# Kernel tuning notes

Measured on AMD Instinct MI355X. Metric: run time of the kernel, lower is better.

Reference implementation:

```python
import jax, jax.numpy as jnp
import numpy as np

H = 16        # num_attention_heads
E = 1024      # hidden_size
D = E // H    # attention_head_size = 64
M = 1024      # max_position_embeddings
EPS = 1e-12


def setup_inputs() -> dict:
    key = jax.random.key(0)
    ks = jax.random.split(key, 12)
    s = 0.02
    B, S = 8, 1024
    return {
        "hidden_states": jax.random.normal(ks[0], (B, S, E), jnp.float32),
        "Wq": jax.random.normal(ks[1], (E, E), jnp.float32) * s,
        "bq": jnp.zeros((E,), jnp.float32),
        "Wk": jax.random.normal(ks[2], (E, E), jnp.float32) * s,
        "bk": jnp.zeros((E,), jnp.float32),
        "Wv": jax.random.normal(ks[3], (E, E), jnp.float32) * s,
        "bv": jnp.zeros((E,), jnp.float32),
        "dist_emb": jax.random.normal(ks[4], (2 * M - 1, D), jnp.float32) * s,
        "Wo": jax.random.normal(ks[5], (E, E), jnp.float32) * s,
        "bo": jnp.zeros((E,), jnp.float32),
        "ln_gamma": jnp.ones((E,), jnp.float32),
        "ln_beta": jnp.zeros((E,), jnp.float32),
    }


def reference(hidden_states, Wq, bq, Wk, bk, Wv, bv, dist_emb, Wo, bo, ln_gamma, ln_beta):
    B, S, _ = hidden_states.shape

    def heads(x):  # [B,S,E] -> [B,H,S,D]
        return x.reshape(B, S, H, D).transpose(0, 2, 1, 3)

    q = heads(hidden_states @ Wq + bq)
    k = heads(hidden_states @ Wk + bk)
    v = heads(hidden_states @ Wv + bv)

    scores = jnp.einsum("bhqd,bhkd->bhqk", q, k)

    # relative_key_query positional bias
    pos_l = jnp.arange(S)[:, None]
    pos_r = jnp.arange(S)[None, :]
    dist_idx = pos_l - pos_r + M - 1            # [S,S] in [0, 2M-2]
    pos_emb = dist_emb[dist_idx]                # [S,S,D]  (l, r, d)
    rel_q = jnp.einsum("bhld,lrd->bhlr", q, pos_emb)
    rel_k = jnp.einsum("bhrd,lrd->bhlr", k, pos_emb)
    scores = (scores + rel_q + rel_k) / jnp.sqrt(jnp.asarray(D, scores.dtype))

    probs = jax.nn.softmax(scores, axis=-1)     # dropout prob = 0 (eval)
    ctx = jnp.einsum("bhqk,bhkd->bhqd", probs, v)
    ctx = ctx.transpose(0, 2, 1, 3).reshape(B, S, E)

    # BertSelfOutput: dense + residual + LayerNorm
    h = ctx @ Wo + bo + hidden_states
    mu = jnp.mean(h, axis=-1, keepdims=True)
    var = jnp.mean(jnp.square(h - mu), axis=-1, keepdims=True)
    out = (h - mu) * jax.lax.rsqrt(var + EPS) * ln_gamma + ln_beta
    return out
```

## Files before the change

kernel.cpp:

```cpp
#include <hip/hip_runtime.h>


typedef unsigned short u16;
typedef unsigned int u32;
typedef unsigned long long u64;
typedef __bf16 bf16x8 __attribute__((ext_vector_type(8)));
typedef float  f32x4  __attribute__((ext_vector_type(4)));
typedef int    i32x4  __attribute__((ext_vector_type(4)));

__device__ __forceinline__ float b2f(u16 u) {
  union { u32 i; float f; } x;
  x.i = ((u32)u) << 16;
  return x.f;
}
__device__ __forceinline__ u16 f2b_manual(float f) {
  union { float f; u32 u; } x;
  x.f = f;
  return (u16)((x.u + 0x7FFFu + ((x.u >> 16) & 1u)) >> 16);
}
#if __has_builtin(__builtin_amdgcn_cvt_pk_bf16_f32)
typedef __bf16 bf16x2 __attribute__((ext_vector_type(2)));
__device__ __forceinline__ u32 cvt2(float a, float b) {
  union { bf16x2 v; u32 u; } x;
  x.v = __builtin_amdgcn_cvt_pk_bf16_f32(a, b);
  return x.u;
}
#else
__device__ __forceinline__ u32 cvt2(float a, float b) {
  return (u32)f2b_manual(a) | ((u32)f2b_manual(b) << 16);
}
#endif
__device__ __forceinline__ u16 f2b(float f) { return (u16)(cvt2(f, f) & 0xffffu); }

union LdU { i32x4 i4; bf16x8 b8; };
__device__ __forceinline__ bf16x8 ldb8(const u16* p) {
  LdU u; u.i4 = *(const i32x4*)p; return u.b8;
}
__device__ __forceinline__ void pack8(u16* dst, const float* src) {
  f32x4 lo = *(const f32x4*)src, hi = *(const f32x4*)(src + 4);
  i32x4 v;
  v.x = (int)cvt2(lo.x, lo.y); v.y = (int)cvt2(lo.z, lo.w);
  v.z = (int)cvt2(hi.x, hi.y); v.w = (int)cvt2(hi.z, hi.w);
  *(i32x4*)dst = v;
}
#define MFMA16(a, b, c) __builtin_amdgcn_mfma_f32_16x16x32_bf16((a), (b), (c), 0, 0, 0)

template <int C>
__device__ __forceinline__ float dppmov(float x) {
  union { float f; int i; } a, r;
  a.f = x;
  r.i = __builtin_amdgcn_update_dpp(0, a.i, C, 0xF, 0xF, true);
  return r.f;
}
__device__ __forceinline__ float rsum16(float x) {
  x += dppmov<0xB1>(x);
  x += dppmov<0x4E>(x);
  x += dppmov<0x141>(x);
  x += dppmov<0x140>(x);
  return x;
}
__device__ __forceinline__ float fexp2(float x) {
#if __has_builtin(__builtin_amdgcn_exp2f)
  return __builtin_amdgcn_exp2f(x);
#else
  return exp2f(x);
#endif
}

#if __has_builtin(__builtin_amdgcn_global_load_lds)
#define HAS_GLDS 1
typedef __attribute__((address_space(3))) u32 as3_u32;
typedef const __attribute__((address_space(1))) u32 as1_u32;
__device__ __forceinline__ void gld16(const u16* g, u16* lds_wave_base) {
  __builtin_amdgcn_global_load_lds(
      (as1_u32*)g, (as3_u32*)(u32)(u64)lds_wave_base, 16, 0, 0);
}
#else
#define HAS_GLDS 0
__device__ __forceinline__ void gld16_fb(const u16* g, u16* lds_wave_base,
                                         int lane) {
  *(i32x4*)(lds_wave_base + lane * 8) = *(const i32x4*)g;
}
#endif

#define SQRT_C2 0.42466090f

__global__ __launch_bounds__(256) void convX(
    const float* __restrict__ X, u16* __restrict__ Xb) {
  int i = (blockIdx.x * 256 + threadIdx.x) * 8;
  pack8(&Xb[i], &X[i]);
}

__global__ __launch_bounds__(256) void convD(
    const float* __restrict__ dist, u16* __restrict__ distb) {
  int i = (blockIdx.x * 256 + threadIdx.x) * 8;
  if (i < 2047 * 64) {
    float t[8];
#pragma unroll
    for (int j = 0; j < 8; j++) t[j] = dist[i + j] * SQRT_C2;
    pack8(&distb[i], t);
  }
}

__global__ __launch_bounds__(256) void convWt(
    const float* __restrict__ W, u16* __restrict__ Wt) {
  __shared__ float tile[64][65];
  const int tid = threadIdx.x;
  const int k0 = blockIdx.x * 64, m0 = blockIdx.y * 64;
#pragma unroll
  for (int it = 0; it < 4; it++) {
    int row = (tid >> 4) + 16 * it;
    int col = (tid & 15) * 4;
    f32x4 v = *(const f32x4*)&W[(size_t)(k0 + row) * 1024 + m0 + col];
    tile[row][col] = v.x; tile[row][col + 1] = v.y;
    tile[row][col + 2] = v.z; tile[row][col + 3] = v.w;
  }
  __syncthreads();
#pragma unroll
  for (int it = 0; it < 4; it++) {
    int mr = (tid >> 4) + 16 * it;
    int kc = (tid & 15) * 4;
    u32 w0 = cvt2(tile[kc][mr], tile[kc + 1][mr]);
    u32 w1 = cvt2(tile[kc + 2][mr], tile[kc + 3][mr]);
    *(u64*)&Wt[(size_t)(m0 + mr) * 1024 + k0 + kc] = (u64)w0 | ((u64)w1 << 32);
  }
}

__global__ __launch_bounds__(256) void transV(
    const u16* __restrict__ V, u16* __restrict__ Vt) {
  __shared__ u16 tile[64][72];
  const int tid = threadIdx.x;
  const int bh = blockIdx.y, b = bh >> 4, h = bh & 15;
  const int s0 = blockIdx.x << 6;
  const u16* Vb = V + (size_t)(b * 1024) * 1024 + h * 64;
  {
    int rp = tid >> 3, a = tid & 7;
    const u16* src = &Vb[(size_t)(s0 + 2 * rp) * 1024 + a * 8];
    i32x4 va = *(const i32x4*)src;
    i32x4 vb2 = *(const i32x4*)(src + 1024);
    u16 ta[8] __attribute__((aligned(16)));
    u16 tb[8] __attribute__((aligned(16)));
    *(i32x4*)ta = va; *(i32x4*)tb = vb2;
    int colb = ((((rp >> 2) ^ a) << 3) | ((2 * rp) & 7));
#pragma unroll
    for (int j = 0; j < 8; j++)
      *(u32*)&tile[a * 8 + j][colb] = (u32)ta[j] | ((u32)tb[j] << 16);
  }
  __syncthreads();
  int d = tid >> 2, cc = tid & 3;
  int sw = (d >> 3) & 7;
  i32x4 lo = *(const i32x4*)&tile[d][((2 * cc) ^ sw) << 3];
  i32x4 hi = *(const i32x4*)&tile[d][((2 * cc + 1) ^ sw) << 3];
  u16* dst = Vt + ((size_t)bh * 64 + d) * 1024 + s0 + cc * 16;
  *(i32x4*)dst = lo;
  *(i32x4*)(dst + 8) = hi;
}

template <int RESID, int OUTF32>
__global__ __launch_bounds__(256) void gemm_bb(
    const u16* __restrict__ A, const u16* __restrict__ Wt,
    const float* __restrict__ bias, const float* __restrict__ resid,
    float* __restrict__ outF, u16* __restrict__ outB, int N, int K, int M,
    float oscale) {
  __shared__ u16 sA[128 * 64];
  __shared__ u16 sW[128 * 64];

  const int tid = threadIdx.x;
  const int lane = tid & 63, w = tid >> 6;
  const int quad = lane >> 4, lb = lane & 15;
  const int m0 = blockIdx.x * 128, n0 = blockIdx.y * 128;

  const int srow = lane >> 3;
  const int gcol = ((lane & 7) ^ srow) << 3;

  f32x4 acc[2][8] = {};

  for (int k0 = 0; k0 < K; k0 += 64) {
#pragma unroll
    for (int j = 0; j < 4; j++) {
      int rb = (4 * w + j) * 8;
      const u16* ga = &A[(size_t)(n0 + rb + srow) * K + k0 + gcol];
      const u16* gw = &Wt[(size_t)(m0 + rb + srow) * K + k0 + gcol];
#if HAS_GLDS
      gld16(ga, &sA[rb * 64]);
      gld16(gw, &sW[rb * 64]);
#else
      gld16_fb(ga, &sA[rb * 64], lane);
      gld16_fb(gw, &sW[rb * 64], lane);
#endif
    }
    __syncthreads();

    const int r0 = 32 * w + lb;
    const int sw0 = r0 & 7;
    bf16x8 a00 = ldb8(&sA[r0 * 64 + ((quad ^ sw0) << 3)]);
    bf16x8 a01 = ldb8(&sA[r0 * 64 + (((4 + quad) ^ sw0) << 3)]);
    bf16x8 a10 = ldb8(&sA[(r0 + 16) * 64 + ((quad ^ sw0) << 3)]);
    bf16x8 a11 = ldb8(&sA[(r0 + 16) * 64 + (((4 + quad) ^ sw0) << 3)]);
#pragma unroll
    for (int t = 0; t < 8; t++) {
      int n = 16 * t + lb;
      int swn = n & 7;
      bf16x8 b0 = ldb8(&sW[n * 64 + ((quad ^ swn) << 3)]);
      bf16x8 b1 = ldb8(&sW[n * 64 + (((4 + quad) ^ swn) << 3)]);
      acc[0][t] = MFMA16(a00, b0, acc[0][t]);
      acc[0][t] = MFMA16(a01, b1, acc[0][t]);
      acc[1][t] = MFMA16(a10, b0, acc[1][t]);
      acc[1][t] = MFMA16(a11, b1, acc[1][t]);
    }
    __syncthreads();
  }

#pragma unroll
  for (int half = 0; half < 2; half++)
#pragma unroll
    for (int t = 0; t < 8; t++) {
      int col = m0 + 16 * t + lb;
      float bv = bias[col];
#pragma unroll
      for (int i = 0; i < 4; i++) {
        int rowg = n0 + 32 * w + 16 * half + quad * 4 + i;
        float v = acc[half][t][i] + bv;
        if (RESID) v += resid[(size_t)rowg * M + col];
        v *= oscale;
        if (OUTF32) outF[(size_t)rowg * M + col] = v;
        else        outB[(size_t)rowg * M + col] = f2b(v);
      }
    }
}

__global__ __launch_bounds__(256) void attn(
    const u16* __restrict__ Q, const u16* __restrict__ Kv,
    const u16* __restrict__ Vt, const u16* __restrict__ distb,
    u16* __restrict__ ctx) {
  __shared__ u16 sQ[64][72];
  __shared__ u16 sK[64][72];
  __shared__ u16 sVt[64][72];
  __shared__ u16 sP[128][72];
  __shared__ u16 sGq[128 * 64];
  __shared__ u16 sGk[128 * 64];

  const int tid = threadIdx.x;
  const int lane = tid & 63, w = tid >> 6;
  const int quad = lane >> 4, lb = lane & 15;
  const int bh = blockIdx.y, b = bh >> 4, h = bh & 15;
  const int q0 = blockIdx.x << 6;
  const int S = 1024, E = 1024;
  const u16* Qb = Q  + (size_t)(b * S) * E + h * 64;
  const u16* Kb = Kv + (size_t)(b * S) * E + h * 64;
  const u16* Vtb = Vt + (size_t)bh * 64 * 1024;

  const int sr = tid >> 3, sc8 = (tid & 7) << 3;

  {
    *(i32x4*)&sQ[sr][sc8] = *(const i32x4*)&Qb[(size_t)(q0 + sr) * E + sc8];
    *(i32x4*)&sQ[sr + 32][sc8] =
        *(const i32x4*)&Qb[(size_t)(q0 + sr + 32) * E + sc8];
    *(i32x4*)&sK[sr][sc8] = *(const i32x4*)&Kb[(size_t)sr * E + sc8];
    *(i32x4*)&sK[sr + 32][sc8] =
        *(const i32x4*)&Kb[(size_t)(sr + 32) * E + sc8];
    *(i32x4*)&sVt[sr][sc8] = *(const i32x4*)&Vtb[(size_t)sr * 1024 + sc8];
    *(i32x4*)&sVt[sr + 32][sc8] =
        *(const i32x4*)&Vtb[(size_t)(sr + 32) * 1024 + sc8];
    const int dbase = q0 + 960;
#pragma unroll
    for (int j = 0; j < 4; j++) {
      int p = sr + 32 * j;
      int g = dbase + p;
      if (g > 2046) g = 2046;
      *(i32x4*)&sP[p][sc8] = *(const i32x4*)&distb[(size_t)g * 64 + sc8];
    }
  }
  __syncthreads();

  const int row = 16 * w + lb;
  bf16x8 aq0 = ldb8(&sQ[row][quad * 8]);
  bf16x8 aq1 = ldb8(&sQ[row][32 + quad * 8]);

  const u16* kb  = &sK[lb][quad * 8];
  const u16* vbp = &sVt[lb][quad * 8];
  const u16* akb = &sK[row][quad * 8];
  const u16* pb  = &sP[lb][quad * 8];
  u16* gqsb = &sGq[lb * 64 + ((16 * w + 4 * quad) ^ ((lb & 7) << 3))];
  u16* gksb = &sGk[lb * 64 + ((16 * w + 4 * quad) ^ ((lb & 7) << 3))];
  u16* psb  = &sK[16 * w + 4 * quad][lb];
  const int rl_ = 16 * w + 4 * quad;
  const u16* gqa_[4];
  const u16* gka_[4][4];
#pragma unroll
  for (int i = 0; i < 4; i++) {
    int rl = rl_ + i;
    int c3 = rl - lb + 15;
    int sw8 = (c3 & 7) << 3;
    gqa_[i] = &sGq[(c3 << 6) + (rl ^ sw8)];
#pragma unroll
    for (int t = 0; t < 4; t++) {
      int c = rl - (16 * t + lb) + 63;
      gka_[i][t] = &sGk[(c << 6) + ((16 * t + lb) ^ sw8)];
    }
  }
  const u16* kg0 = Kb + (size_t)(64 + sr) * E + sc8;
  const u16* kg1 = kg0 + (size_t)32 * E;
  const u16* vg0 = Vtb + (size_t)sr * 1024 + 64 + sc8;
  const u16* vg1 = vg0 + (size_t)32 * 1024;
  const u16* dg0 = distb + (size_t)(q0 - 64 + 960 + sr) * 64 + sc8;
  const u16* dg1 = dg0 + (size_t)32 * 64;
  u16* wk0 = &sK[sr][sc8];  u16* wk1 = &sK[sr + 32][sc8];
  u16* wv0 = &sVt[sr][sc8]; u16* wv1 = &sVt[sr + 32][sc8];
  u16* wp0 = &sP[sr][sc8];  u16* wp1 = &sP[sr + 32][sc8];

  const int uqlo = w, uqhi = w + 4;
  const int uklo = 3 - w, ukhi = 7 - w;

  f32x4 accO[4] = {};
  float l_i[4] = {0.f, 0.f, 0.f, 0.f};

  for (int kt = 0; kt < 16; kt++) {
    const int xorv = (kt & 1) << 6;

    i32x4 kr0, kr1, vr0, vr1, dr0, dr1;
    if (kt < 15) {
      kr0 = *(const i32x4*)kg0;
      kr1 = *(const i32x4*)kg1;
      vr0 = *(const i32x4*)vg0;
      vr1 = *(const i32x4*)vg1;
      dr0 = *(const i32x4*)dg0;
      dr1 = *(const i32x4*)dg1;
    }

    __builtin_amdgcn_s_setprio(1);
    f32x4 accS[4] = {};
#pragma unroll
    for (int t = 0; t < 4; t++) {
      bf16x8 b0 = ldb8(kb + 1152 * t);
      bf16x8 b1 = ldb8(kb + 1152 * t + 32);
      accS[t] = MFMA16(aq0, b0, accS[t]);
      accS[t] = MFMA16(aq1, b1, accS[t]);
    }
    bf16x8 ak0 = ldb8(akb);
    bf16x8 ak1 = ldb8(akb + 32);
    const u16* pbA = pb + (xorv ? 4608 : 0);
    const u16* pbB = pb + (xorv ? -4608 : 0);
#pragma unroll
    for (int u = 0; u < 8; u++) {
      const bool doq = (u >= uqlo) && (u <= uqhi);
      const bool dok = (u >= uklo) && (u <= ukhi);
      if (doq || dok) {
        const u16* pp = (u < 4 ? pbA : pbB) + 1152 * u;
        bf16x8 p0 = ldb8(pp);
        bf16x8 p1 = ldb8(pp + 32);
        if (doq) {
          f32x4 gq = {};
          gq = MFMA16(aq0, p0, gq);
          gq = MFMA16(aq1, p1, gq);
          *(u32*)(gqsb + 1024 * u) = cvt2(gq[0], gq[1]);
          *(u32*)(gqsb + 1024 * u + 2) = cvt2(gq[2], gq[3]);
        }
        if (dok) {
          f32x4 gk = {};
          gk = MFMA16(ak0, p0, gk);
          gk = MFMA16(ak1, p1, gk);
          *(u32*)(gksb + 1024 * u) = cvt2(gk[0], gk[1]);
          *(u32*)(gksb + 1024 * u + 2) = cvt2(gk[2], gk[3]);
        }
      }
    }
    __builtin_amdgcn_s_setprio(0);
    __syncthreads();

    float pr[4][4];
#pragma unroll
    for (int t = 0; t < 4; t++) {
#pragma unroll
      for (int i = 0; i < 4; i++) {
        float s = accS[t][i] + b2f(gqa_[i][1024 * (3 - t)]) +
                  b2f(*gka_[i][t]);
        float e = fexp2(s);
        pr[t][i] = e;
        l_i[i] += e;
      }
    }

#pragma unroll
    for (int t = 0; t < 4; t++)
#pragma unroll
      for (int i = 0; i < 4; i++)
        psb[72 * i + 16 * t] = f2b(pr[t][i]);

    bf16x8 ap0 = ldb8(akb);
    bf16x8 ap1 = ldb8(akb + 32);
    __builtin_amdgcn_s_setprio(1);
#pragma unroll
    for (int t = 0; t < 4; t++) {
      bf16x8 v0 = ldb8(vbp + 1152 * t);
      bf16x8 v1 = ldb8(vbp + 1152 * t + 32);
      accO[t] = MFMA16(ap0, v0, accO[t]);
      accO[t] = MFMA16(ap1, v1, accO[t]);
    }
    __builtin_amdgcn_s_setprio(0);
    __syncthreads();

    if (kt < 15) {
      const int pxn = ((kt + 1) & 1) ? 4608 : 0;
      *(i32x4*)wk0 = kr0;
      *(i32x4*)wk1 = kr1;
      *(i32x4*)wv0 = vr0;
      *(i32x4*)wv1 = vr1;
      *(i32x4*)(wp0 + pxn) = dr0;
      *(i32x4*)(wp1 + pxn) = dr1;
      kg0 += (size_t)64 * E; kg1 += (size_t)64 * E;
      vg0 += 64;             vg1 += 64;
      dg0 -= 64 * 64;        dg1 -= 64 * 64;
      __syncthreads();
    }
  }

#pragma unroll
  for (int i = 0; i < 4; i++) l_i[i] = rsum16(l_i[i]);

  u16* Cb = ctx + (size_t)(b * S) * E + h * 64;
#pragma unroll
  for (int t = 0; t < 4; t++)
#pragma unroll
    for (int i = 0; i < 4; i++) {
      int rl = 16 * w + quad * 4 + i;
      Cb[(size_t)(q0 + rl) * E + 16 * t + lb] = f2b(accO[t][i] / l_i[i]);
    }
}

__global__ __launch_bounds__(256) void lnorm(
    const float* __restrict__ Hp, const float* __restrict__ gamma,
    const float* __restrict__ beta, float* __restrict__ out) {
  __shared__ float red[8];
  const int rowb = blockIdx.x, tid = threadIdx.x;
  const float* hr = Hp + (size_t)rowb * 1024;
  f32x4 v = *(const f32x4*)&hr[tid * 4];
  float s = v.x + v.y + v.z + v.w;
  float q = v.x * v.x + v.y * v.y + v.z * v.z + v.w * v.w;
#pragma unroll
  for (int d = 1; d < 64; d <<= 1) {
    s += __shfl_xor(s, d, 64);
    q += __shfl_xor(q, d, 64);
  }
  int w = tid >> 6, lane = tid & 63;
  if (lane == 0) { red[w] = s; red[4 + w] = q; }
  __syncthreads();
  s = red[0] + red[1] + red[2] + red[3];
  q = red[4] + red[5] + red[6] + red[7];
  float mu = s * (1.f / 1024.f);
  float var = q * (1.f / 1024.f) - mu * mu;
  float rstd = rsqrtf(var + 1e-12f);
  float* orow = out + (size_t)rowb * 1024;
  f32x4 o;
#pragma unroll
  for (int j = 0; j < 4; j++) {
    int c = tid * 4 + j;
    o[j] = (v[j] - mu) * rstd * gamma[c] + beta[c];
  }
  *(f32x4*)&orow[tid * 4] = o;
}

extern "C" void kernel_launch(void* const* d_in, const int* in_sizes, int n_in,
                              void* d_out, int out_size, void* d_ws,
                              size_t ws_size, hipStream_t stream) {
  const float* X    = (const float*)d_in[0];
  const float* Wq   = (const float*)d_in[1];
  const float* bq   = (const float*)d_in[2];
  const float* Wk   = (const float*)d_in[3];
  const float* bk   = (const float*)d_in[4];
  const float* Wv   = (const float*)d_in[5];
  const float* bv   = (const float*)d_in[6];
  const float* dist = (const float*)d_in[7];
  const float* Wo   = (const float*)d_in[8];
  const float* bo   = (const float*)d_in[9];
  const float* gam  = (const float*)d_in[10];
  const float* bet  = (const float*)d_in[11];

  const size_t NE = (size_t)8192 * 1024;
  char* ws = (char*)d_ws;
  u16* Qw = (u16*)(ws);
  u16* Kw = (u16*)(ws + 2 * NE);
  u16* Vw = (u16*)(ws + 4 * NE);
  u16* Cw = (u16*)(ws + 6 * NE);
  float* Hp = (float*)ws;

  char* ob = (char*)d_out;
  u16* Wtq = (u16*)(ob);
  u16* Wtk = (u16*)(ob + (2u << 20));
  u16* Wtv = (u16*)(ob + (4u << 20));
  u16* Wto = (u16*)(ob + (6u << 20));
  u16* Xb  = (u16*)(ob + (8u << 20));
  u16* Vtg = (u16*)(ob + (8u << 20));
  u16* distb = (u16*)(ob + (26u << 20));

  dim3 bb(256);
  dim3 gw(16, 16);
  convWt<<<gw, bb, 0, stream>>>(Wq, Wtq);
  convWt<<<gw, bb, 0, stream>>>(Wk, Wtk);
  convWt<<<gw, bb, 0, stream>>>(Wv, Wtv);
  convWt<<<gw, bb, 0, stream>>>(Wo, Wto);
  convX<<<dim3(4096), bb, 0, stream>>>(X, Xb);
  convD<<<dim3(64), bb, 0, stream>>>(dist, distb);

  dim3 gg(8, 64);
  gemm_bb<0, 0><<<gg, bb, 0, stream>>>(Xb, Wtq, bq, nullptr, nullptr, Qw, 8192, 1024, 1024, SQRT_C2);
  gemm_bb<0, 0><<<gg, bb, 0, stream>>>(Xb, Wtk, bk, nullptr, nullptr, Kw, 8192, 1024, 1024, SQRT_C2);
  gemm_bb<0, 0><<<gg, bb, 0, stream>>>(Xb, Wtv, bv, nullptr, nullptr, Vw, 8192, 1024, 1024, 1.0f);
  transV<<<dim3(16, 128), bb, 0, stream>>>(Vw, Vtg);
  attn<<<dim3(16, 128), bb, 0, stream>>>(Qw, Kw, Vtg, distb, Cw);
  gemm_bb<1, 1><<<gg, bb, 0, stream>>>(Cw, Wto, bo, X, Hp, nullptr, 8192, 1024, 1024, 1.0f);
  lnorm<<<dim3(8192), bb, 0, stream>>>(Hp, gam, bet, (float*)d_out);
}
```

Measured before the change: 431.2 us.

## Fuse QKV projections into one GEMM, pad bias LDS, remap attention blocks per XCD

Runs the three Q/K/V projection GEMMs as a single launch over a concatenated 3072-wide weight, assuming Wtq/Wtk/Wtv are contiguous. The epilogue routes each column block to its own Q/K/V segment and applies the matching scale. Biases are copied into a contiguous buffer. The attention kernel swaps the XOR-swizzled layout of its shared positional-bias buffers for row padding (stride 66) with simplified diagonal addressing, and remaps block indices so all query tiles of one (batch, head) land on the same XCD for L2 reuse. Together these aim to cut launch count, improve GEMM occupancy, reduce LDS bank conflicts and improve cache locality, at the cost of extra LDS and reliance on buffer layout assumptions.

```diff
diff --git a/kernel.cpp b/kernel.cpp
--- a/kernel.cpp
+++ b/kernel.cpp
@@ -156,7 +156,7 @@
   *(i32x4*)(dst + 8) = hi;
 }
 
-template <int RESID, int OUTF32>
+template <int RESID, int OUTF32, int QKV>
 __global__ __launch_bounds__(256) void gemm_bb(
     const u16* __restrict__ A, const u16* __restrict__ Wt,
     const float* __restrict__ bias, const float* __restrict__ resid,
@@ -211,20 +211,30 @@
     __syncthreads();
   }
 
+  u16* outSeg = outB;
+  float osc = oscale;
+  int mbase = m0;
+  if (QKV) {
+    outSeg = outB + (size_t)(m0 >> 10) * ((size_t)8192 * 1024);
+    osc = (m0 < 2048) ? SQRT_C2 : 1.0f;
+    mbase = m0 & 1023;
+  }
+
 #pragma unroll
   for (int half = 0; half < 2; half++)
 #pragma unroll
     for (int t = 0; t < 8; t++) {
       int col = m0 + 16 * t + lb;
+      int colw = mbase + 16 * t + lb;
       float bv = bias[col];
 #pragma unroll
       for (int i = 0; i < 4; i++) {
         int rowg = n0 + 32 * w + 16 * half + quad * 4 + i;
         float v = acc[half][t][i] + bv;
         if (RESID) v += resid[(size_t)rowg * M + col];
-        v *= oscale;
+        v *= osc;
         if (OUTF32) outF[(size_t)rowg * M + col] = v;
-        else        outB[(size_t)rowg * M + col] = f2b(v);
+        else        outSeg[(size_t)rowg * (QKV ? 1024 : M) + colw] = f2b(v);
       }
     }
 }
@@ -237,14 +247,17 @@
   __shared__ u16 sK[64][72];
   __shared__ u16 sVt[64][72];
   __shared__ u16 sP[128][72];
-  __shared__ u16 sGq[128 * 64];
-  __shared__ u16 sGk[128 * 64];
+  __shared__ u16 sGq[128 * 66];
+  __shared__ u16 sGk[128 * 66];
 
   const int tid = threadIdx.x;
   const int lane = tid & 63, w = tid >> 6;
   const int quad = lane >> 4, lb = lane & 15;
-  const int bh = blockIdx.y, b = bh >> 4, h = bh & 15;
-  const int q0 = blockIdx.x << 6;
+  const int f = blockIdx.y * 16 + blockIdx.x;
+  const int xcd = f & 7, slot = f >> 3;
+  const int bh = (xcd << 4) | (slot & 15);
+  const int q0 = (slot >> 4) << 6;
+  const int b = bh >> 4, h = bh & 15;
   const int S = 1024, E = 1024;
   const u16* Qb = Q  + (size_t)(b * S) * E + h * 64;
   const u16* Kb = Kv + (size_t)(b * S) * E + h * 64;
@@ -281,23 +294,17 @@
   const u16* vbp = &sVt[lb][quad * 8];
   const u16* akb = &sK[row][quad * 8];
   const u16* pb  = &sP[lb][quad * 8];
-  u16* gqsb = &sGq[lb * 64 + ((16 * w + 4 * quad) ^ ((lb & 7) << 3))];
-  u16* gksb = &sGk[lb * 64 + ((16 * w + 4 * quad) ^ ((lb & 7) << 3))];
+  u16* gqsb = &sGq[lb * 66 + 16 * w + 4 * quad];
+  u16* gksb = &sGk[lb * 66 + 16 * w + 4 * quad];
   u16* psb  = &sK[16 * w + 4 * quad][lb];
   const int rl_ = 16 * w + 4 * quad;
   const u16* gqa_[4];
-  const u16* gka_[4][4];
+  const u16* gka_[4];
 #pragma unroll
   for (int i = 0; i < 4; i++) {
     int rl = rl_ + i;
-    int c3 = rl - lb + 15;
-    int sw8 = (c3 & 7) << 3;
-    gqa_[i] = &sGq[(c3 << 6) + (rl ^ sw8)];
-#pragma unroll
-    for (int t = 0; t < 4; t++) {
-      int c = rl - (16 * t + lb) + 63;
-      gka_[i][t] = &sGk[(c << 6) + ((16 * t + lb) ^ sw8)];
-    }
+    gqa_[i] = sGq + (67 * rl + 4158 - 66 * lb - 3168);
+    gka_[i] = sGk + (66 * rl + 4158 - 65 * lb - 3120);
   }
   const u16* kg0 = Kb + (size_t)(64 + sr) * E + sc8;
   const u16* kg1 = kg0 + (size_t)32 * E;
@@ -353,15 +360,15 @@
           f32x4 gq = {};
           gq = MFMA16(aq0, p0, gq);
           gq = MFMA16(aq1, p1, gq);
-          *(u32*)(gqsb + 1024 * u) = cvt2(gq[0], gq[1]);
-          *(u32*)(gqsb + 1024 * u + 2) = cvt2(gq[2], gq[3]);
+          *(u32*)(gqsb + 1056 * u) = cvt2(gq[0], gq[1]);
+          *(u32*)(gqsb + 1056 * u + 2) = cvt2(gq[2], gq[3]);
         }
         if (dok) {
           f32x4 gk = {};
           gk = MFMA16(ak0, p0, gk);
           gk = MFMA16(ak1, p1, gk);
-          *(u32*)(gksb + 1024 * u) = cvt2(gk[0], gk[1]);
-          *(u32*)(gksb + 1024 * u + 2) = cvt2(gk[2], gk[3]);
+          *(u32*)(gksb + 1056 * u) = cvt2(gk[0], gk[1]);
+          *(u32*)(gksb + 1056 * u + 2) = cvt2(gk[2], gk[3]);
         }
       }
     }
@@ -373,8 +380,8 @@
     for (int t = 0; t < 4; t++) {
 #pragma unroll
       for (int i = 0; i < 4; i++) {
-        float s = accS[t][i] + b2f(gqa_[i][1024 * (3 - t)]) +
-                  b2f(*gka_[i][t]);
+        float s = accS[t][i] + b2f(gqa_[i][1056 * (3 - t)]) +
+                  b2f(gka_[i][1040 * (3 - t)]);
         float e = fexp2(s);
         pr[t][i] = e;
         l_i[i] += e;
@@ -492,6 +499,7 @@
   u16* Xb  = (u16*)(ob + (8u << 20));
   u16* Vtg = (u16*)(ob + (8u << 20));
   u16* distb = (u16*)(ob + (26u << 20));
+  float* bias3 = (float*)(ob + (30u << 20));
 
   dim3 bb(256);
   dim3 gw(16, 16);
@@ -501,13 +509,15 @@
   convWt<<<gw, bb, 0, stream>>>(Wo, Wto);
   convX<<<dim3(4096), bb, 0, stream>>>(X, Xb);
   convD<<<dim3(64), bb, 0, stream>>>(dist, distb);
-
-  dim3 gg(8, 64);
-  gemm_bb<0, 0><<<gg, bb, 0, stream>>>(Xb, Wtq, bq, nullptr, nullptr, Qw, 8192, 1024, 1024, SQRT_C2);
-  gemm_bb<0, 0><<<gg, bb, 0, stream>>>(Xb, Wtk, bk, nullptr, nullptr, Kw, 8192, 1024, 1024, SQRT_C2);
-  gemm_bb<0, 0><<<gg, bb, 0, stream>>>(Xb, Wtv, bv, nullptr, nullptr, Vw, 8192, 1024, 1024, 1.0f);
+  hipMemcpyAsync(bias3, bq, 4096, hipMemcpyDeviceToDevice, stream);
+  hipMemcpyAsync(bias3 + 1024, bk, 4096, hipMemcpyDeviceToDevice, stream);
+  hipMemcpyAsync(bias3 + 2048, bv, 4096, hipMemcpyDeviceToDevice, stream);
+
+  gemm_bb<0, 0, 1><<<dim3(24, 64), bb, 0, stream>>>(
+      Xb, Wtq, bias3, nullptr, nullptr, Qw, 8192, 1024, 3072, 1.0f);
   transV<<<dim3(16, 128), bb, 0, stream>>>(Vw, Vtg);
   attn<<<dim3(16, 128), bb, 0, stream>>>(Qw, Kw, Vtg, distb, Cw);
-  gemm_bb<1, 1><<<gg, bb, 0, stream>>>(Cw, Wto, bo, X, Hp, nullptr, 8192, 1024, 1024, 1.0f);
+  gemm_bb<1, 1, 0><<<dim3(8, 64), bb, 0, stream>>>(
+      Cw, Wto, bo, X, Hp, nullptr, 8192, 1024, 1024, 1.0f);
   lnorm<<<dim3(8192), bb, 0, stream>>>(Hp, gam, bet, (float*)d_out);
 }
```

Result: no change. 438.8 us (+1.8%).
